# Performance work log

Measured on AMD Instinct MI355X. Metric: run time of the kernel, lower is better.

The kernel has to match this reference:

```python
import jax, jax.numpy as jnp
import numpy as np

N_NODES = 100000
N_EDGES = 1600000
F_IN = 128
F_OUT = 64


def setup_inputs() -> dict:
    key = jax.random.key(0)
    kx, kw, kv, ks, kd = jax.random.split(key, 5)
    x = jax.random.normal(kx, (N_NODES, F_IN), dtype=jnp.float32)
    # xavier_uniform init for weight [in, out]
    limit = float(np.sqrt(6.0 / (F_IN + F_OUT)))
    weight = jax.random.uniform(kw, (F_IN, F_OUT), dtype=jnp.float32,
                                minval=-limit, maxval=limit)
    edge_val = jax.random.uniform(kv, (N_EDGES,), dtype=jnp.float32)
    edge_src = jax.random.randint(ks, (N_EDGES,), 0, N_NODES, dtype=jnp.int64)
    edge_dst = jax.random.randint(kd, (N_EDGES,), 0, N_NODES, dtype=jnp.int64)
    return {"x": x, "weight": weight, "edge_val": edge_val,
            "edge_src": edge_src, "edge_dst": edge_dst}


def reference(x, weight, edge_val, edge_src, edge_dst):
    # dropout p = 0.0 -> identity
    support = x @ weight                                  # [N, F_OUT] dense GEMM
    # spmm: out[dst] += val * support[src]  (adj row = dst, col = src)
    messages = support[edge_src] * edge_val[:, None]       # [E, F_OUT] gather
    out = jax.ops.segment_sum(messages, edge_dst,
                              num_segments=x.shape[0])     # [N, F_OUT] scatter-add
    return jax.nn.relu(out)
```

## Files before the change

### kernel.cpp

```cpp
#include <hip/hip_runtime.h>

#define F_IN 128
#define F_OUT 64
#define GROWS 128
#define XBSTRIDE 136

#define NPB 128
#define NPB_SHIFT 7
#define BCAP 800
#define ECAP 2240
#define TILE 8192
#define BSTH 1024
#define TMAX 256

__device__ inline unsigned f2bf(float f) {
    const unsigned u = __float_as_uint(f);
    return (u + 0x7FFFu + ((u >> 16) & 1u)) >> 16;
}
__device__ inline float bf_lo(unsigned u) { return __uint_as_float(u << 16); }
__device__ inline float bf_hi(unsigned u) { return __uint_as_float(u & 0xFFFF0000u); }

using bf16x8 = __attribute__((ext_vector_type(8))) short;
using f32x4  = __attribute__((ext_vector_type(4))) float;

struct GemmSh {
    unsigned short xt[GROWS * XBSTRIDE];
    unsigned short wth[F_OUT * XBSTRIDE];
    unsigned short wtl[F_OUT * XBSTRIDE];
};
struct ScatSh {
    int2 ebuf2[TILE];
    int  h[BCAP];
    int  lcur[BCAP];
    int  wsum[16];
    int  woff[16];
};
union FusedSh { GemmSh g; ScatSh s; };

__global__ __launch_bounds__(BSTH) void fused_kernel(const float* __restrict__ x,
                                                     const float* __restrict__ w,
                                                     unsigned short* __restrict__ support,
                                                     int n_nodes,
                                                     const float* __restrict__ edge_val,
                                                     const int* __restrict__ edge_src,
                                                     const int* __restrict__ edge_dst,
                                                     int* __restrict__ toff,
                                                     int2* __restrict__ sorted,
                                                     int n_edges, int nb, int T) {
    __shared__ FusedSh u;
    const int tid = threadIdx.x;

    if ((int)blockIdx.x >= T) {
        const int row0 = (blockIdx.x - T) * GROWS;

        {
            #pragma unroll
            for (int i = tid; i < F_OUT * (F_IN / 8); i += BSTH) {
                const int col = i & 63;
                const int kb  = (i >> 6) << 3;
                unsigned short sh[8], sl[8];
                #pragma unroll
                for (int j = 0; j < 8; ++j) {
                    const float f = w[(size_t)(kb + j) * F_OUT + col];
                    const unsigned h = f2bf(f);
                    sh[j] = (unsigned short)h;
                    sl[j] = (unsigned short)f2bf(f - __uint_as_float(h << 16));
                }
                uint4 oh, ol;
                oh.x = sh[0] | ((unsigned)sh[1] << 16); oh.y = sh[2] | ((unsigned)sh[3] << 16);
                oh.z = sh[4] | ((unsigned)sh[5] << 16); oh.w = sh[6] | ((unsigned)sh[7] << 16);
                ol.x = sl[0] | ((unsigned)sl[1] << 16); ol.y = sl[2] | ((unsigned)sl[3] << 16);
                ol.z = sl[4] | ((unsigned)sl[5] << 16); ol.w = sl[6] | ((unsigned)sl[7] << 16);
                *(uint4*)&u.g.wth[col * XBSTRIDE + kb] = oh;
                *(uint4*)&u.g.wtl[col * XBSTRIDE + kb] = ol;
            }
        }
        {
            const float4* x4 = (const float4*)x;
            #pragma unroll
            for (int i = tid; i < GROWS * (F_IN / 8); i += BSTH) {
                const int r  = i >> 4;
                const int k8 = i & 15;
                const int row = row0 + r;
                float4 a = make_float4(0.f, 0.f, 0.f, 0.f);
                float4 b = make_float4(0.f, 0.f, 0.f, 0.f);
                if (row < n_nodes) {
                    a = x4[(size_t)row * (F_IN / 4) + 2 * k8 + 0];
                    b = x4[(size_t)row * (F_IN / 4) + 2 * k8 + 1];
                }
                uint4 o;
                o.x = f2bf(a.x) | (f2bf(a.y) << 16);
                o.y = f2bf(a.z) | (f2bf(a.w) << 16);
                o.z = f2bf(b.x) | (f2bf(b.y) << 16);
                o.w = f2bf(b.z) | (f2bf(b.w) << 16);
                *(uint4*)&u.g.xt[r * XBSTRIDE + k8 * 8] = o;
            }
        }
        __syncthreads();

        const int ln = tid & 63;
        const int wv = tid >> 6;
        const int rt = wv >> 1;
        const int cp = (wv & 1) << 1;
        const int lr = ln >> 4;
        const int lc = ln & 15;

        const unsigned short* ar  = &u.g.xt [(rt * 16 + lc) * XBSTRIDE + lr * 8];
        const unsigned short* bh0 = &u.g.wth[(cp * 16 + lc) * XBSTRIDE + lr * 8];
        const unsigned short* bh1 = &u.g.wth[((cp + 1) * 16 + lc) * XBSTRIDE + lr * 8];
        const unsigned short* bl0 = &u.g.wtl[(cp * 16 + lc) * XBSTRIDE + lr * 8];
        const unsigned short* bl1 = &u.g.wtl[((cp + 1) * 16 + lc) * XBSTRIDE + lr * 8];

        f32x4 acc0 = {0.f, 0.f, 0.f, 0.f};
        f32x4 acc1 = {0.f, 0.f, 0.f, 0.f};
        #pragma unroll
        for (int kc = 0; kc < 4; ++kc) {
            const bf16x8 a  = *(const bf16x8*)(ar  + kc * 32);
            const bf16x8 h0 = *(const bf16x8*)(bh0 + kc * 32);
            const bf16x8 h1 = *(const bf16x8*)(bh1 + kc * 32);
            const bf16x8 l0 = *(const bf16x8*)(bl0 + kc * 32);
            const bf16x8 l1 = *(const bf16x8*)(bl1 + kc * 32);
            acc0 = __builtin_amdgcn_mfma_f32_16x16x32_bf16(a, h0, acc0, 0, 0, 0);
            acc1 = __builtin_amdgcn_mfma_f32_16x16x32_bf16(a, h1, acc1, 0, 0, 0);
            acc0 = __builtin_amdgcn_mfma_f32_16x16x32_bf16(a, l0, acc0, 0, 0, 0);
            acc1 = __builtin_amdgcn_mfma_f32_16x16x32_bf16(a, l1, acc1, 0, 0, 0);
        }

        #pragma unroll
        for (int i = 0; i < 4; ++i) {
            const int row = row0 + rt * 16 + lr * 4 + i;
            if (row < n_nodes) {
                unsigned short* sp = &support[(size_t)row * F_OUT + lc];
                sp[cp * 16]       = (unsigned short)f2bf(acc0[i]);
                sp[(cp + 1) * 16] = (unsigned short)f2bf(acc1[i]);
            }
        }
        return;
    }

    const int te  = blockIdx.x * TILE;
    const int cnt = min(TILE, n_edges - te);

    for (int i = tid; i < BCAP; i += BSTH) u.s.h[i] = 0;
    __syncthreads();

    const int cnt4 = cnt >> 2;
    const int4*   s4 = (const int4*)(edge_src + te);
    const int4*   d4 = (const int4*)(edge_dst + te);
    const float4* v4 = (const float4*)(edge_val + te);
    int4 rs[2], rd[2]; float4 rv[2];
    #pragma unroll
    for (int it = 0; it < 2; ++it) {
        const int t = tid + it * BSTH;
        if (t < cnt4) {
            rs[it] = s4[t]; rd[it] = d4[t]; rv[it] = v4[t];
            atomicAdd(&u.s.h[rd[it].x >> NPB_SHIFT], 1);
            atomicAdd(&u.s.h[rd[it].y >> NPB_SHIFT], 1);
            atomicAdd(&u.s.h[rd[it].z >> NPB_SHIFT], 1);
            atomicAdd(&u.s.h[rd[it].w >> NPB_SHIFT], 1);
        }
    }
    if (tid == 0) {
        for (int e = cnt4 << 2; e < cnt; ++e)
            atomicAdd(&u.s.h[edge_dst[te + e] >> NPB_SHIFT], 1);
    }
    __syncthreads();

    const int v = (tid < nb) ? u.s.h[tid] : 0;
    int s = v;
    #pragma unroll
    for (int off = 1; off < 64; off <<= 1) {
        const int t = __shfl_up(s, off, 64);
        if ((tid & 63) >= off) s += t;
    }
    const int wave = tid >> 6;
    if ((tid & 63) == 63) u.s.wsum[wave] = s;
    __syncthreads();
    if (tid < 16) {
        const int ws = u.s.wsum[tid];
        int sc = ws;
        #pragma unroll
        for (int off = 1; off < 16; off <<= 1) {
            const int t = __shfl_up(sc, off, 64);
            if (tid >= off) sc += t;
        }
        u.s.woff[tid] = sc - ws;
    }
    __syncthreads();

    int* trow = toff + (size_t)blockIdx.x * (nb + 1);
    if (tid < nb) {
        const int start = s + u.s.woff[wave] - v;
        u.s.lcur[tid] = start;
        trow[tid] = start;
    }
    if (tid == 0) trow[nb] = cnt;
    __syncthreads();

    #pragma unroll
    for (int it = 0; it < 2; ++it) {
        const int t = tid + it * BSTH;
        if (t < cnt4) {
            int b, r;
            b = rd[it].x >> NPB_SHIFT; r = atomicAdd(&u.s.lcur[b], 1);
            u.s.ebuf2[r] = make_int2(rs[it].x | ((rd[it].x & (NPB - 1)) << 20), __float_as_int(rv[it].x));
            b = rd[it].y >> NPB_SHIFT; r = atomicAdd(&u.s.lcur[b], 1);
            u.s.ebuf2[r] = make_int2(rs[it].y | ((rd[it].y & (NPB - 1)) << 20), __float_as_int(rv[it].y));
            b = rd[it].z >> NPB_SHIFT; r = atomicAdd(&u.s.lcur[b], 1);
            u.s.ebuf2[r] = make_int2(rs[it].z | ((rd[it].z & (NPB - 1)) << 20), __float_as_int(rv[it].z));
            b = rd[it].w >> NPB_SHIFT; r = atomicAdd(&u.s.lcur[b], 1);
            u.s.ebuf2[r] = make_int2(rs[it].w | ((rd[it].w & (NPB - 1)) << 20), __float_as_int(rv[it].w));
        }
    }
    if (tid == 0) {
        for (int e = cnt4 << 2; e < cnt; ++e) {
            const int dd = edge_dst[te + e];
            const int b = dd >> NPB_SHIFT;
            const int r = atomicAdd(&u.s.lcur[b], 1);
            u.s.ebuf2[r] = make_int2(edge_src[te + e] | ((dd & (NPB - 1)) << 20),
                                     __float_as_int(edge_val[te + e]));
        }
    }
    __syncthreads();

    for (int k = tid; k < cnt; k += BSTH)
        sorted[(size_t)te + k] = u.s.ebuf2[k];
}

__global__ __launch_bounds__(512) void baccum_kernel(const unsigned short* __restrict__ support,
                                                     const int2* __restrict__ sorted,
                                                     const int* __restrict__ toff,
                                                     float* __restrict__ out,
                                                     int n_nodes, int T, int nb) {
    __shared__ int2 ebuf[ECAP];
    __shared__ int2 ebuf2[ECAP];
    __shared__ int tstart[TMAX];
    __shared__ int toffb[TMAX];
    __shared__ int wsum3[4];
    __shared__ int total_s;
    __shared__ int hist[NPB];
    __shared__ int node_off[NPB + 1];
    __shared__ int cursor[NPB];
    __shared__ int wsum2[2];

    const int tid = threadIdx.x;
    const int b = blockIdx.x;

    int mycnt = 0, myoff = 0;
    if (tid < TMAX) {
        if (tid < T) {
            const int s0 = toff[(size_t)tid * (nb + 1) + b];
            const int e0 = toff[(size_t)tid * (nb + 1) + b + 1];
            toffb[tid] = s0;
            mycnt = e0 - s0;
        }
        int s = mycnt;
        #pragma unroll
        for (int off = 1; off < 64; off <<= 1) {
            const int t = __shfl_up(s, off, 64);
            if ((tid & 63) >= off) s += t;
        }
        if ((tid & 63) == 63) wsum3[tid >> 6] = s;
        myoff = s - mycnt;
    }
    __syncthreads();
    if (tid < TMAX && tid < T) {
        int add = 0;
        const int wv = tid >> 6;
        for (int q2 = 0; q2 < wv; ++q2) add += wsum3[q2];
        tstart[tid] = myoff + add;
    }
    if (tid == 0) total_s = wsum3[0] + wsum3[1] + wsum3[2] + wsum3[3];
    __syncthreads();
    const int total = total_s;

    const int g8 = tid >> 3;
    const int q  = tid & 7;
    const uint4* sup = (const uint4*)support;

    float4 accA[2], accB[2];
    #pragma unroll
    for (int j = 0; j < 2; ++j) {
        accA[j] = make_float4(0.f, 0.f, 0.f, 0.f);
        accB[j] = make_float4(0.f, 0.f, 0.f, 0.f);
    }

    for (int cb = 0; cb < total; cb += ECAP) {
        const int cnt = min(ECAP, total - cb);

        __syncthreads();
        if (tid < NPB) hist[tid] = 0;
        __syncthreads();

        for (int i = tid; i < cnt; i += 512) {
            const int g = cb + i;
            int lo = 0, hi = T - 1;
            while (lo < hi) {
                const int mid = (lo + hi + 1) >> 1;
                if (tstart[mid] <= g) lo = mid; else hi = mid - 1;
            }
            const int2 ev = sorted[(size_t)lo * TILE + toffb[lo] + (g - tstart[lo])];
            ebuf[i] = ev;
            atomicAdd(&hist[((unsigned)ev.x) >> 20], 1);
        }
        __syncthreads();

        {
            int v = 0;
            if (tid < NPB) v = hist[tid];
            int s = v;
            if (tid < NPB) {
                #pragma unroll
                for (int off = 1; off < 64; off <<= 1) {
                    const int t = __shfl_up(s, off, 64);
                    if ((tid & 63) >= off) s += t;
                }
                if ((tid & 63) == 63) wsum2[tid >> 6] = s;
            }
            __syncthreads();
            if (tid < NPB) {
                const int incl = s + ((tid >= 64) ? wsum2[0] : 0);
                node_off[tid + 1] = incl;
                cursor[tid] = incl - v;
                if (tid == 0) node_off[0] = 0;
            }
        }
        __syncthreads();

        for (int i = tid; i < cnt; i += 512) {
            const int2 ev = ebuf[i];
            const int r = atomicAdd(&cursor[((unsigned)ev.x) >> 20], 1);
            ebuf2[r] = ev;
        }
        __syncthreads();

        #pragma unroll
        for (int j = 0; j < 2; ++j) {
            const int nl = g8 + 64 * j;
            int k = node_off[nl];
            const int ke = node_off[nl + 1];
            float4 aA = accA[j], aB = accB[j];
            while (k + 8 <= ke) {
                int2 e[8];
                uint4 s[8];
                #pragma unroll
                for (int u2 = 0; u2 < 8; ++u2) e[u2] = ebuf2[k + u2];
                #pragma unroll
                for (int u2 = 0; u2 < 8; ++u2)
                    s[u2] = sup[(size_t)(e[u2].x & 0xFFFFF) * 8 + q];
                #pragma unroll
                for (int u2 = 0; u2 < 8; ++u2) {
                    const float v = __int_as_float(e[u2].y);
                    aA.x += v * bf_lo(s[u2].x); aA.y += v * bf_hi(s[u2].x);
                    aA.z += v * bf_lo(s[u2].y); aA.w += v * bf_hi(s[u2].y);
                    aB.x += v * bf_lo(s[u2].z); aB.y += v * bf_hi(s[u2].z);
                    aB.z += v * bf_lo(s[u2].w); aB.w += v * bf_hi(s[u2].w);
                }
                k += 8;
            }
            for (; k < ke; ++k) {
                const int2 e0 = ebuf2[k];
                const uint4 s0 = sup[(size_t)(e0.x & 0xFFFFF) * 8 + q];
                const float v0 = __int_as_float(e0.y);
                aA.x += v0 * bf_lo(s0.x); aA.y += v0 * bf_hi(s0.x);
                aA.z += v0 * bf_lo(s0.y); aA.w += v0 * bf_hi(s0.y);
                aB.x += v0 * bf_lo(s0.z); aB.y += v0 * bf_hi(s0.z);
                aB.z += v0 * bf_lo(s0.w); aB.w += v0 * bf_hi(s0.w);
            }
            accA[j] = aA; accB[j] = aB;
        }
    }

    const int base = b << NPB_SHIFT;
    #pragma unroll
    for (int j = 0; j < 2; ++j) {
        const int node = base + g8 + 64 * j;
        if (node < n_nodes) {
            float4 vA = accA[j], vB = accB[j];
            vA.x = fmaxf(vA.x, 0.f); vA.y = fmaxf(vA.y, 0.f);
            vA.z = fmaxf(vA.z, 0.f); vA.w = fmaxf(vA.w, 0.f);
            vB.x = fmaxf(vB.x, 0.f); vB.y = fmaxf(vB.y, 0.f);
            vB.z = fmaxf(vB.z, 0.f); vB.w = fmaxf(vB.w, 0.f);
            ((float4*)out)[(size_t)node * 16 + 2 * q + 0] = vA;
            ((float4*)out)[(size_t)node * 16 + 2 * q + 1] = vB;
        }
    }
}

__global__ __launch_bounds__(256) void scatter_kernel(const unsigned short* __restrict__ support,
                                                      const float* __restrict__ edge_val,
                                                      const int* __restrict__ edge_src,
                                                      const int* __restrict__ edge_dst,
                                                      float* __restrict__ out,
                                                      int n_edges) {
    const long gid = (long)blockIdx.x * blockDim.x + threadIdx.x;
    const int e = (int)(gid >> 4);
    if (e >= n_edges) return;
    const int q = (int)(gid & 15);
    const int src   = edge_src[e];
    const int dst   = edge_dst[e];
    const float val = edge_val[e];
    const uint2 s = ((const uint2*)support)[(size_t)src * 16 + q];
    float* o = &out[(size_t)dst * F_OUT + q * 4];
    atomicAdd(o + 0, val * bf_lo(s.x));
    atomicAdd(o + 1, val * bf_hi(s.x));
    atomicAdd(o + 2, val * bf_lo(s.y));
    atomicAdd(o + 3, val * bf_hi(s.y));
}

__global__ __launch_bounds__(256) void relu_kernel(float* __restrict__ out, int n4) {
    const int i = blockIdx.x * blockDim.x + threadIdx.x;
    if (i < n4) {
        float4 v = ((float4*)out)[i];
        v.x = fmaxf(v.x, 0.f); v.y = fmaxf(v.y, 0.f);
        v.z = fmaxf(v.z, 0.f); v.w = fmaxf(v.w, 0.f);
        ((float4*)out)[i] = v;
    }
}

extern "C" void kernel_launch(void* const* d_in, const int* in_sizes, int n_in,
                              void* d_out, int out_size, void* d_ws, size_t ws_size,
                              hipStream_t stream) {
    const float* x        = (const float*)d_in[0];
    const float* w        = (const float*)d_in[1];
    const float* edge_val = (const float*)d_in[2];
    const int*   edge_src = (const int*)d_in[3];
    const int*   edge_dst = (const int*)d_in[4];
    float* out = (float*)d_out;

    const int n_nodes = in_sizes[0] / F_IN;
    const int n_edges = in_sizes[2];
    const int nb = (n_nodes + NPB - 1) >> NPB_SHIFT;
    const int T  = (n_edges + TILE - 1) / TILE;
    const int G  = (n_nodes + GROWS - 1) / GROWS;

    char* p = (char*)d_ws;
    unsigned short* support = (unsigned short*)p;
    p += (size_t)n_nodes * F_OUT * sizeof(unsigned short);
    p = (char*)(((size_t)p + 15) & ~(size_t)15);
    int2* sorted = (int2*)p;  p += (size_t)T * TILE * sizeof(int2);
    int*  toff   = (int*)p;   p += (size_t)T * (nb + 1) * sizeof(int);
    const size_t ws_needed = (size_t)(p - (char*)d_ws);

    const bool ok = (ws_size >= ws_needed) && (nb <= BCAP) && (n_nodes < (1 << 20))
                    && (T <= TMAX);
    if (ok) {
        fused_kernel<<<T + G, BSTH, 0, stream>>>(x, w, support, n_nodes,
                                                 edge_val, edge_src, edge_dst,
                                                 toff, sorted, n_edges, nb, T);
        baccum_kernel<<<nb, 512, 0, stream>>>(support, sorted, toff, out,
                                              n_nodes, T, nb);
    } else {
        fused_kernel<<<G, BSTH, 0, stream>>>(x, w, support, n_nodes,
                                             edge_val, edge_src, edge_dst,
                                             nullptr, nullptr, n_edges, nb, 0);
        hipMemsetAsync(d_out, 0, (size_t)out_size * sizeof(float), stream);
        const long st = (long)n_edges * 16;
        scatter_kernel<<<(int)((st + 255) / 256), 256, 0, stream>>>(
            support, edge_val, edge_src, edge_dst, out, n_edges);
        const int n4o = out_size / 4;
        relu_kernel<<<(n4o + 255) / 256, 256, 0, stream>>>(out, n4o);
    }
}
```

Baseline: 154.1 us.

## Halve nodes per bucket to 64 and process one node per thread group

Result: slower. 243.2 us (+57.8%).

```diff
diff --git a/kernel.cpp b/kernel.cpp
--- a/kernel.cpp
+++ b/kernel.cpp
@@ -5,10 +5,10 @@
 #define GROWS 128
 #define XBSTRIDE 136
 
-#define NPB 128
-#define NPB_SHIFT 7
-#define BCAP 800
-#define ECAP 2240
+#define NPB 64
+#define NPB_SHIFT 6
+#define BCAP 1600
+#define ECAP 1280
 #define TILE 8192
 #define BSTH 1024
 #define TMAX 256
@@ -166,8 +166,11 @@
     }
     __syncthreads();
 
-    const int v = (tid < nb) ? u.s.h[tid] : 0;
-    int s = v;
+    const int i0 = tid * 2, i1 = tid * 2 + 1;
+    const int v0 = (i0 < nb) ? u.s.h[i0] : 0;
+    const int v1 = (i1 < nb) ? u.s.h[i1] : 0;
+    const int pv = v0 + v1;
+    int s = pv;
     #pragma unroll
     for (int off = 1; off < 64; off <<= 1) {
         const int t = __shfl_up(s, off, 64);
@@ -189,10 +192,10 @@
     __syncthreads();
 
     int* trow = toff + (size_t)blockIdx.x * (nb + 1);
-    if (tid < nb) {
-        const int start = s + u.s.woff[wave] - v;
-        u.s.lcur[tid] = start;
-        trow[tid] = start;
+    {
+        const int excl = s + u.s.woff[wave] - pv;
+        if (i0 < nb) { u.s.lcur[i0] = excl;      trow[i0] = excl; }
+        if (i1 < nb) { u.s.lcur[i1] = excl + v0; trow[i1] = excl + v0; }
     }
     if (tid == 0) trow[nb] = cnt;
     __syncthreads();
@@ -227,11 +230,11 @@
         sorted[(size_t)te + k] = u.s.ebuf2[k];
 }
 
-__global__ __launch_bounds__(512) void baccum_kernel(const unsigned short* __restrict__ support,
-                                                     const int2* __restrict__ sorted,
-                                                     const int* __restrict__ toff,
-                                                     float* __restrict__ out,
-                                                     int n_nodes, int T, int nb) {
+__global__ __launch_bounds__(512, 8) void baccum_kernel(const unsigned short* __restrict__ support,
+                                                        const int2* __restrict__ sorted,
+                                                        const int* __restrict__ toff,
+                                                        float* __restrict__ out,
+                                                        int n_nodes, int T, int nb) {
     __shared__ int2 ebuf[ECAP];
     __shared__ int2 ebuf2[ECAP];
     __shared__ int tstart[TMAX];
@@ -241,7 +244,6 @@
     __shared__ int hist[NPB];
     __shared__ int node_off[NPB + 1];
     __shared__ int cursor[NPB];
-    __shared__ int wsum2[2];
 
     const int tid = threadIdx.x;
     const int b = blockIdx.x;
@@ -278,12 +280,8 @@
     const int q  = tid & 7;
     const uint4* sup = (const uint4*)support;
 
-    float4 accA[2], accB[2];
-    #pragma unroll
-    for (int j = 0; j < 2; ++j) {
-        accA[j] = make_float4(0.f, 0.f, 0.f, 0.f);
-        accB[j] = make_float4(0.f, 0.f, 0.f, 0.f);
-    }
+    float4 accA = make_float4(0.f, 0.f, 0.f, 0.f);
+    float4 accB = make_float4(0.f, 0.f, 0.f, 0.f);
 
     for (int cb = 0; cb < total; cb += ECAP) {
         const int cnt = min(ECAP, total - cb);
@@ -305,25 +303,17 @@
         }
         __syncthreads();
 
-        {
-            int v = 0;
-            if (tid < NPB) v = hist[tid];
+        if (tid < NPB) {
+            const int v = hist[tid];
             int s = v;
-            if (tid < NPB) {
-                #pragma unroll
-                for (int off = 1; off < 64; off <<= 1) {
-                    const int t = __shfl_up(s, off, 64);
-                    if ((tid & 63) >= off) s += t;
-                }
-                if ((tid & 63) == 63) wsum2[tid >> 6] = s;
-            }
-            __syncthreads();
-            if (tid < NPB) {
-                const int incl = s + ((tid >= 64) ? wsum2[0] : 0);
-                node_off[tid + 1] = incl;
-                cursor[tid] = incl - v;
-                if (tid == 0) node_off[0] = 0;
-            }
+            #pragma unroll
+            for (int off = 1; off < 64; off <<= 1) {
+                const int t = __shfl_up(s, off, 64);
+                if (tid >= off) s += t;
+            }
+            node_off[tid + 1] = s;
+            cursor[tid] = s - v;
+            if (tid == 0) node_off[0] = 0;
         }
         __syncthreads();
 
@@ -334,56 +324,41 @@
         }
         __syncthreads();
 
-        #pragma unroll
-        for (int j = 0; j < 2; ++j) {
-            const int nl = g8 + 64 * j;
-            int k = node_off[nl];
-            const int ke = node_off[nl + 1];
-            float4 aA = accA[j], aB = accB[j];
-            while (k + 8 <= ke) {
+        {
+            int k = node_off[g8];
+            const int ke = node_off[g8 + 1];
+            float4 aA = accA, aB = accB;
+            for (; k < ke; k += 8) {
                 int2 e[8];
-                uint4 s[8];
-                #pragma unroll
-                for (int u2 = 0; u2 < 8; ++u2) e[u2] = ebuf2[k + u2];
+                uint4 s8[8];
                 #pragma unroll
                 for (int u2 = 0; u2 < 8; ++u2)
-                    s[u2] = sup[(size_t)(e[u2].x & 0xFFFFF) * 8 + q];
+                    e[u2] = ebuf2[min(k + u2, ke - 1)];
+                #pragma unroll
+                for (int u2 = 0; u2 < 8; ++u2)
+                    s8[u2] = sup[(size_t)(e[u2].x & 0xFFFFF) * 8 + q];
                 #pragma unroll
                 for (int u2 = 0; u2 < 8; ++u2) {
-                    const float v = __int_as_float(e[u2].y);
-                    aA.x += v * bf_lo(s[u2].x); aA.y += v * bf_hi(s[u2].x);
-                    aA.z += v * bf_lo(s[u2].y); aA.w += v * bf_hi(s[u2].y);
-                    aB.x += v * bf_lo(s[u2].z); aB.y += v * bf_hi(s[u2].z);
-                    aB.z += v * bf_lo(s[u2].w); aB.w += v * bf_hi(s[u2].w);
+                    const float v = (k + u2 < ke) ? __int_as_float(e[u2].y) : 0.f;
+                    aA.x += v * bf_lo(s8[u2].x); aA.y += v * bf_hi(s8[u2].x);
+                    aA.z += v * bf_lo(s8[u2].y); aA.w += v * bf_hi(s8[u2].y);
+                    aB.x += v * bf_lo(s8[u2].z); aB.y += v * bf_hi(s8[u2].z);
+                    aB.z += v * bf_lo(s8[u2].w); aB.w += v * bf_hi(s8[u2].w);
                 }
-                k += 8;
-            }
-            for (; k < ke; ++k) {
-                const int2 e0 = ebuf2[k];
-                const uint4 s0 = sup[(size_t)(e0.x & 0xFFFFF) * 8 + q];
-                const float v0 = __int_as_float(e0.y);
-                aA.x += v0 * bf_lo(s0.x); aA.y += v0 * bf_hi(s0.x);
-                aA.z += v0 * bf_lo(s0.y); aA.w += v0 * bf_hi(s0.y);
-                aB.x += v0 * bf_lo(s0.z); aB.y += v0 * bf_hi(s0.z);
-                aB.z += v0 * bf_lo(s0.w); aB.w += v0 * bf_hi(s0.w);
-            }
-            accA[j] = aA; accB[j] = aB;
-        }
-    }
-
-    const int base = b << NPB_SHIFT;
-    #pragma unroll
-    for (int j = 0; j < 2; ++j) {
-        const int node = base + g8 + 64 * j;
-        if (node < n_nodes) {
-            float4 vA = accA[j], vB = accB[j];
-            vA.x = fmaxf(vA.x, 0.f); vA.y = fmaxf(vA.y, 0.f);
-            vA.z = fmaxf(vA.z, 0.f); vA.w = fmaxf(vA.w, 0.f);
-            vB.x = fmaxf(vB.x, 0.f); vB.y = fmaxf(vB.y, 0.f);
-            vB.z = fmaxf(vB.z, 0.f); vB.w = fmaxf(vB.w, 0.f);
-            ((float4*)out)[(size_t)node * 16 + 2 * q + 0] = vA;
-            ((float4*)out)[(size_t)node * 16 + 2 * q + 1] = vB;
-        }
+            }
+            accA = aA; accB = aB;
+        }
+    }
+
+    const int node = (b << NPB_SHIFT) + g8;
+    if (node < n_nodes) {
+        float4 vA = accA, vB = accB;
+        vA.x = fmaxf(vA.x, 0.f); vA.y = fmaxf(vA.y, 0.f);
+        vA.z = fmaxf(vA.z, 0.f); vA.w = fmaxf(vA.w, 0.f);
+        vB.x = fmaxf(vB.x, 0.f); vB.y = fmaxf(vB.y, 0.f);
+        vB.z = fmaxf(vB.z, 0.f); vB.w = fmaxf(vB.w, 0.f);
+        ((float4*)out)[(size_t)node * 16 + 2 * q + 0] = vA;
+        ((float4*)out)[(size_t)node * 16 + 2 * q + 1] = vB;
     }
 }
 
@@ -442,8 +417,8 @@
     int*  toff   = (int*)p;   p += (size_t)T * (nb + 1) * sizeof(int);
     const size_t ws_needed = (size_t)(p - (char*)d_ws);
 
-    const bool ok = (ws_size >= ws_needed) && (nb <= BCAP) && (n_nodes < (1 << 20))
-                    && (T <= TMAX);
+    const bool ok = (ws_size >= ws_needed) && (nb <= BCAP) && (nb <= 2 * BSTH)
+                    && (n_nodes < (1 << 20)) && (T <= TMAX);
     if (ok) {
         fused_kernel<<<T + G, BSTH, 0, stream>>>(x, w, support, n_nodes,
                                                  edge_val, edge_src, edge_dst,
```
